# Optimization experiments

Hardware: AMD Instinct MI355X
Metric: run time of the kernel (lower is better)

The kernel has to match this reference:

```python
import jax, jax.numpy as jnp
import numpy as np

LEAK = 0.3          # config['leak_rate']
LAST_N = 8          # config['last_n_outputs']


def setup_inputs() -> dict:
    key = jax.random.key(0)
    k1, k2, k3, k4, k5 = jax.random.split(key, 5)
    B, T, F, H, O = 256, 1000, 64, 1024, 10
    x = jax.random.normal(k1, (B, T, F), dtype=jnp.float32)
    w_in = jax.random.normal(k2, (F, H), dtype=jnp.float32) * 0.2
    # reservoir matrix scaled to spectral radius ~0.9 (randn HxH has radius ~sqrt(H))
    w_r = jax.random.normal(k3, (H, H), dtype=jnp.float32) * (0.9 / np.sqrt(H))
    w_lin = jax.random.normal(k4, (O, H * LAST_N), dtype=jnp.float32) * 0.02
    b_lin = jax.random.normal(k5, (O,), dtype=jnp.float32) * 0.02
    return {"x": x, "w_in": w_in, "w_r": w_r, "w_lin": w_lin, "b_lin": b_lin}


def _esn_forward(x, w_in, w_r, w_lin, b_lin):
    B, T, F = x.shape
    H = w_in.shape[1]
    n = LAST_N
    # t = 0: h_0 = h_hat (no leaky combine per original code)
    h = jnp.tanh(x[:, 0, :] @ w_in)

    def step(h, xt):
        h_hat = jnp.tanh(xt @ w_in + h @ w_r)
        return (1.0 - LEAK) * h + LEAK * h_hat

    # steps 1 .. T-n-1: carry only, no outputs stored
    def body_nohist(h, xt):
        return step(h, xt), None

    xs_mid = jnp.swapaxes(x[:, 1:T - n, :], 0, 1)   # [T-n-1, B, F]
    h, _ = jax.lax.scan(body_nohist, h, xs_mid)

    # steps T-n .. T-1: keep states (out_list in original)
    def body_hist(h, xt):
        h = step(h, xt)
        return h, h

    xs_tail = jnp.swapaxes(x[:, T - n:, :], 0, 1)   # [n, B, F]
    _, hs = jax.lax.scan(body_hist, h, xs_tail)     # [n, B, H]

    # torch.cat(out_list, dim=1): oldest kept state first -> [B, n*H]
    feats = jnp.transpose(hs, (1, 0, 2)).reshape(B, n * H)
    return feats @ w_lin.T + b_lin


def reference(x, w_in, w_r, w_lin, b_lin):
    return _esn_forward(x, w_in, w_r, w_lin, b_lin)
```

## Files before the change

kernel.cpp:

```cpp
#include <hip/hip_runtime.h>
#include <math.h>

#define LEAK   0.3f
#define ONEML  0.7f

typedef unsigned short u16;
typedef unsigned int   u32;
typedef unsigned long long u64;
typedef __attribute__((ext_vector_type(4))) float f32x4;
typedef __attribute__((ext_vector_type(8))) short s16x8;

constexpr int B = 256, T = 1000, F = 64, H = 1024, O = 10, NTAIL = 8;
constexpr int TSTART  = T - NTAIL;
constexpr int KS      = 34;
constexpr int PSTRIDE = 1096;


constexpr size_t OFF_PACKED = 0;
constexpr size_t OFF_HGL    = 0x240000;
constexpr size_t OFF_FLAGS  = 0x340000;
constexpr size_t OFF_FEATS  = 0x344000;

__device__ __forceinline__ u16 f2bf(float f) {
  union { float f; u32 u; } v; v.f = f;
  u32 r = v.u + 0x7fffu + ((v.u >> 16) & 1u);
  return (u16)(r >> 16);
}

__device__ __forceinline__ float ftanh(float s) {
  const float sc = fminf(fmaxf(s, -9.0f), 9.0f);
  const float e2 = __builtin_amdgcn_exp2f(sc * 2.8853900817779268f);
  return 1.0f - 2.0f * __builtin_amdgcn_rcpf(e2 + 1.0f);
}

__global__ void esn_pack(const float* __restrict__ w_in, const float* __restrict__ w_r,
                         u16* __restrict__ packed) {
  int gid = blockIdx.x * 256 + threadIdx.x;
  if (gid >= 64 * KS * 64) return;
  int lane = gid & 63;
  int ks   = (gid >> 6) % KS;
  int nt   = gid / (KS * 64);
  int n    = nt * 16 + (lane & 15);
  int g    = lane >> 4;
  u16 v[8];
  #pragma unroll
  for (int jj = 0; jj < 8; ++jj) {
    int kk = 8 * g + jj;
    float w;
    if (ks < 2) w = w_in[(ks * 32 + kk) * H + n];
    else        w = w_r[((ks - 2) * 32 + kk) * H + n];
    v[jj] = f2bf(w);
  }
  u64* dst = (u64*)(packed + (size_t)gid * 8);
  dst[0] = ((const u64*)v)[0];
  dst[1] = ((const u64*)v)[1];
}

__global__ __launch_bounds__(512, 1) void esn_recur(const float* __restrict__ x,
    const u16* __restrict__ packed, u16* __restrict__ hgl,
    u32* __restrict__ flags, float* __restrict__ feats) {
  __shared__ u16 panel[2][16][PSTRIDE];
  __shared__ u16 forcepad[6144];

  const int tid  = threadIdx.x;
  const int lane = tid & 63, wv = tid >> 6;
  const int ci   = blockIdx.x >> 3;
  const int cj   = blockIdx.x & 7;
  const int g    = lane >> 4, m16 = lane & 15;
  const int nt   = cj * 8 + wv;
  const int cc   = nt * 16 + m16;
  const int bbase = ci * 16;
  const bool ownCols = ((tid >> 6) == cj);

  s16x8 bfrag[KS];
  #pragma unroll
  for (int ks = 0; ks < KS; ++ks)
    bfrag[ks] = *(const s16x8*)(packed + (((size_t)nt * KS + ks) * 64 + lane) * 8);

  float hreg[4] = {0.f, 0.f, 0.f, 0.f};

  for (int t = 0; t < T; ++t) {
    const int buf = t & 1;
    const int nb  = buf ^ 1;

    {
      const int r = tid >> 5;
      const int c = (tid & 31) * 2;
      const float2 v = *(const float2*)(x + (((size_t)(bbase + r)) * T + t) * (size_t)F + c);
      u16 o[2] = { f2bf(v.x), f2bf(v.y) };
      *(u32*)&panel[buf][r][c] = *(const u32*)o;
    }

    if (t > 0) {
      const u32 target = (u32)t;
      u32* fp = &flags[ci * 64 + lane];
      int guard = 0;
      for (;;) {
        u32 fv = __hip_atomic_load(fp, __ATOMIC_RELAXED, __HIP_MEMORY_SCOPE_AGENT);
        if (__all((int)(fv >= target))) break;
        if (++guard > (1 << 16)) break;
      }
      asm volatile("" ::: "memory");
    }

    if (t == 0) {
      #pragma unroll
      for (int it = 0; it < 16; ++it)
        *(u32*)&panel[buf][it][64 + tid * 2] = 0u;
    } else if (!ownCols) {
      const int pb = (t + 1) & 1;
      u32 vb[16];
      #pragma unroll
      for (int it = 0; it < 16; ++it)
        vb[it] = __hip_atomic_load(
            (const u32*)(hgl + ((((size_t)pb * 16 + ci) * 16 + it) * H + tid * 2)),
            __ATOMIC_RELAXED, __HIP_MEMORY_SCOPE_AGENT);
      #pragma unroll
      for (int it = 0; it < 16; ++it)
        *(u32*)&panel[buf][it][64 + tid * 2] = vb[it];
    }
    __syncthreads();

    f32x4 acc0 = {0.f,0.f,0.f,0.f}, acc1 = {0.f,0.f,0.f,0.f};
    #pragma unroll
    for (int ks = 0; ks < KS; ++ks) {
      s16x8 a = *(const s16x8*)&panel[buf][m16][ks * 32 + g * 8];
      if (ks & 1) acc1 = __builtin_amdgcn_mfma_f32_16x16x32_bf16(a, bfrag[ks], acc1, 0, 0, 0);
      else        acc0 = __builtin_amdgcn_mfma_f32_16x16x32_bf16(a, bfrag[ks], acc0, 0, 0, 0);
    }

    #pragma unroll
    for (int r = 0; r < 4; ++r) {
      const float s  = acc0[r] + acc1[r];
      const float th = ftanh(s);
      const float hn = (t == 0) ? th : (ONEML * hreg[r] + LEAK * th);
      hreg[r] = hn;
      const int rr = g * 4 + r;
      panel[nb][rr][64 + cc] = f2bf(hn);
      if (t >= TSTART)
        feats[((size_t)(bbase + rr)) * (H * NTAIL) + (t - TSTART) * H + cc] = hn;
    }

    asm volatile("s_waitcnt lgkmcnt(0)" ::: "memory");
    {
      const int r  = lane >> 2;
      const int c4 = (lane & 3) * 4;
      const u64 v = *(const u64*)&panel[nb][r][64 + nt * 16 + c4];
      __hip_atomic_store(
          (u64*)(hgl + ((((size_t)buf * 16 + ci) * 16 + r) * H + nt * 16 + c4)),
          v, __ATOMIC_RELAXED, __HIP_MEMORY_SCOPE_AGENT);
    }

    asm volatile("s_waitcnt vmcnt(0)" ::: "memory");
    if (lane == 0)
      __hip_atomic_store(&flags[ci * 64 + nt], (u32)(t + 1),
                         __ATOMIC_RELAXED, __HIP_MEMORY_SCOPE_AGENT);
  }
  if (tid == 511) ((volatile u16*)forcepad)[0] = (u16)lane;
}

__global__ __launch_bounds__(256) void esn_out(const float* __restrict__ feats,
    const float* __restrict__ w_lin, const float* __restrict__ b_lin,
    float* __restrict__ out) {
  const int b = blockIdx.x;
  const int tid = threadIdx.x;
  const int lane = tid & 63, wv = tid >> 6;
  float p[O];
  #pragma unroll
  for (int o = 0; o < O; ++o) p[o] = 0.f;
  const float* fr = feats + (size_t)b * (H * NTAIL);
  for (int idx = tid; idx < H * NTAIL; idx += 256) {
    const float f = fr[idx];
    #pragma unroll
    for (int o = 0; o < O; ++o) p[o] += f * w_lin[o * (H * NTAIL) + idx];
  }
  __shared__ float red[O][4];
  #pragma unroll
  for (int o = 0; o < O; ++o) {
    float v = p[o];
    for (int off = 32; off > 0; off >>= 1) v += __shfl_down(v, off);
    if (lane == 0) red[o][wv] = v;
  }
  __syncthreads();
  if (tid < O)
    out[b * O + tid] = red[tid][0] + red[tid][1] + red[tid][2] + red[tid][3] + b_lin[tid];
}

extern "C" void kernel_launch(void* const* d_in, const int* in_sizes, int n_in,
                              void* d_out, int out_size, void* d_ws, size_t ws_size,
                              hipStream_t stream) {
  const float* x     = (const float*)d_in[0];
  const float* w_in  = (const float*)d_in[1];
  const float* w_r   = (const float*)d_in[2];
  const float* w_lin = (const float*)d_in[3];
  const float* b_lin = (const float*)d_in[4];
  char* ws = (char*)d_ws;
  u16* packed = (u16*)(ws + OFF_PACKED);
  u16* hgl    = (u16*)(ws + OFF_HGL);
  u32* flags  = (u32*)(ws + OFF_FLAGS);
  float* feats= (float*)(ws + OFF_FEATS);
  float* out  = (float*)d_out;

  hipMemsetAsync(flags, 0, 4096 * sizeof(u32), stream);
  esn_pack<<<(64 * KS * 64 + 255) / 256, 256, 0, stream>>>(w_in, w_r, packed);

  void* args[] = { (void*)&x, (void*)&packed, (void*)&hgl, (void*)&flags, (void*)&feats };
  hipLaunchCooperativeKernel((void*)esn_recur, dim3(128), dim3(512), args, 0, stream);

  esn_out<<<B, 256, 0, stream>>>(feats, w_lin, b_lin, out);
}
```

Measured before the change: 3.425 ms.

## Embed step tags in exchanged hidden-state words and drop separate flag barrier

Each bf16 hidden value is now stored in a 32-bit word together with a 16-bit step tag. Consumers spin directly on the data loads until every tag matches the expected step. This removes the separate flag array, the memset, the vmcnt wait before the flag store, and the flag-polling round trip, fusing data and signal into one transfer. In exchange, the exchanged data doubles in size, spins now reload full data vectors, and the guard is smaller. Stale workspace contents could also spuriously match a tag, since the buffer is no longer cleared.

```diff
diff --git a/kernel.cpp b/kernel.cpp
--- a/kernel.cpp
+++ b/kernel.cpp
@@ -17,9 +17,8 @@
 
 
 constexpr size_t OFF_PACKED = 0;
-constexpr size_t OFF_HGL    = 0x240000;
-constexpr size_t OFF_FLAGS  = 0x340000;
-constexpr size_t OFF_FEATS  = 0x344000;
+constexpr size_t OFF_HGL    = 0x220000;
+constexpr size_t OFF_FEATS  = 0x420000;
 
 __device__ __forceinline__ u16 f2bf(float f) {
   union { float f; u32 u; } v; v.f = f;
@@ -57,8 +56,7 @@
 }
 
 __global__ __launch_bounds__(512, 1) void esn_recur(const float* __restrict__ x,
-    const u16* __restrict__ packed, u16* __restrict__ hgl,
-    u32* __restrict__ flags, float* __restrict__ feats) {
+    const u16* __restrict__ packed, u32* __restrict__ hgl, float* __restrict__ feats) {
   __shared__ u16 panel[2][16][PSTRIDE];
   __shared__ u16 forcepad[6144];
 
@@ -91,33 +89,39 @@
       *(u32*)&panel[buf][r][c] = *(const u32*)o;
     }
 
-    if (t > 0) {
-      const u32 target = (u32)t;
-      u32* fp = &flags[ci * 64 + lane];
-      int guard = 0;
-      for (;;) {
-        u32 fv = __hip_atomic_load(fp, __ATOMIC_RELAXED, __HIP_MEMORY_SCOPE_AGENT);
-        if (__all((int)(fv >= target))) break;
-        if (++guard > (1 << 16)) break;
-      }
-      asm volatile("" ::: "memory");
-    }
-
     if (t == 0) {
       #pragma unroll
       for (int it = 0; it < 16; ++it)
         *(u32*)&panel[buf][it][64 + tid * 2] = 0u;
-    } else if (!ownCols) {
+    } else {
+      const u32 st = (u32)t;
       const int pb = (t + 1) & 1;
-      u32 vb[16];
-      #pragma unroll
-      for (int it = 0; it < 16; ++it)
-        vb[it] = __hip_atomic_load(
-            (const u32*)(hgl + ((((size_t)pb * 16 + ci) * 16 + it) * H + tid * 2)),
-            __ATOMIC_RELAXED, __HIP_MEMORY_SCOPE_AGENT);
-      #pragma unroll
-      for (int it = 0; it < 16; ++it)
-        *(u32*)&panel[buf][it][64 + tid * 2] = vb[it];
+      const u32* base = hgl + (((size_t)pb * 16 + ci) * 16) * H + tid * 2;
+      u64 vb[16];
+      int guard = 0;
+      for (;;) {
+        bool ok = true;
+        if (!ownCols) {
+          #pragma unroll
+          for (int it = 0; it < 16; ++it)
+            vb[it] = __hip_atomic_load((const u64*)(base + (size_t)it * H),
+                                       __ATOMIC_RELAXED, __HIP_MEMORY_SCOPE_AGENT);
+          #pragma unroll
+          for (int it = 0; it < 16; ++it)
+            ok &= ((((u32)vb[it]) & 0xffffu) == st) &&
+                  ((((u32)(vb[it] >> 32)) & 0xffffu) == st);
+        }
+        if (__all((int)ok)) break;
+        if (++guard > 4096) break;
+      }
+      if (!ownCols) {
+        #pragma unroll
+        for (int it = 0; it < 16; ++it) {
+          u16 o[2] = { (u16)(((u32)vb[it]) >> 16), (u16)(((u32)(vb[it] >> 32)) >> 16) };
+          *(u32*)&panel[buf][it][64 + tid * 2] = *(const u32*)o;
+        }
+      }
+      asm volatile("" ::: "memory");
     }
     __syncthreads();
 
@@ -145,16 +149,18 @@
     {
       const int r  = lane >> 2;
       const int c4 = (lane & 3) * 4;
-      const u64 v = *(const u64*)&panel[nb][r][64 + nt * 16 + c4];
-      __hip_atomic_store(
-          (u64*)(hgl + ((((size_t)buf * 16 + ci) * 16 + r) * H + nt * 16 + c4)),
-          v, __ATOMIC_RELAXED, __HIP_MEMORY_SCOPE_AGENT);
-    }
-
-    asm volatile("s_waitcnt vmcnt(0)" ::: "memory");
-    if (lane == 0)
-      __hip_atomic_store(&flags[ci * 64 + nt], (u32)(t + 1),
+      const u64 two = *(const u64*)&panel[nb][r][64 + nt * 16 + c4];
+      const u32 st  = (u32)(t + 1);
+      const u32 w0 = (((u32)(two       & 0xffffu)) << 16) | st;
+      const u32 w1 = (((u32)((two>>16) & 0xffffu)) << 16) | st;
+      const u32 w2 = (((u32)((two>>32) & 0xffffu)) << 16) | st;
+      const u32 w3 = (((u32)((two>>48) & 0xffffu)) << 16) | st;
+      u32* gp = hgl + (((size_t)buf * 16 + ci) * 16 + r) * H + nt * 16 + c4;
+      __hip_atomic_store((u64*)gp,       (((u64)w1) << 32) | w0,
                          __ATOMIC_RELAXED, __HIP_MEMORY_SCOPE_AGENT);
+      __hip_atomic_store((u64*)(gp + 2), (((u64)w3) << 32) | w2,
+                         __ATOMIC_RELAXED, __HIP_MEMORY_SCOPE_AGENT);
+    }
   }
   if (tid == 511) ((volatile u16*)forcepad)[0] = (u16)lane;
 }
@@ -196,15 +202,13 @@
   const float* b_lin = (const float*)d_in[4];
   char* ws = (char*)d_ws;
   u16* packed = (u16*)(ws + OFF_PACKED);
-  u16* hgl    = (u16*)(ws + OFF_HGL);
-  u32* flags  = (u32*)(ws + OFF_FLAGS);
+  u32* hgl    = (u32*)(ws + OFF_HGL);
   float* feats= (float*)(ws + OFF_FEATS);
   float* out  = (float*)d_out;
 
-  hipMemsetAsync(flags, 0, 4096 * sizeof(u32), stream);
   esn_pack<<<(64 * KS * 64 + 255) / 256, 256, 0, stream>>>(w_in, w_r, packed);
 
-  void* args[] = { (void*)&x, (void*)&packed, (void*)&hgl, (void*)&flags, (void*)&feats };
+  void* args[] = { (void*)&x, (void*)&packed, (void*)&hgl, (void*)&feats };
   hipLaunchCooperativeKernel((void*)esn_recur, dim3(128), dim3(512), args, 0, stream);
 
   esn_out<<<B, 256, 0, stream>>>(feats, w_lin, b_lin, out);
```

After: 4.064 ms. 1.19x slower.
